# Kernel tuning notes

Hardware: AMD Instinct MI355X
Metric: run time of the kernel (lower is better)

The kernel has to match this reference:

```python
import jax, jax.numpy as jnp
import numpy as np

B, D, M, R, C = 1024, 32, 8, 4096, 32
TOPK_P = 0.1  # hard-coded in torch forward
EPS = 1e-9


def setup_inputs() -> dict:
    key = jax.random.key(0)
    k0, k1, k2, k3, k4 = jax.random.split(key, 5)
    x = jax.random.normal(k0, (B, D), dtype=jnp.float32)
    centers = jax.random.normal(k1, (D, M), dtype=jnp.float32)
    # widths kept away from 0 so gaussian MFs don't all underflow
    widths = jax.random.uniform(k2, (D, M), dtype=jnp.float32, minval=0.5, maxval=1.5)
    consequents = jax.random.uniform(k3, (R, D + 1, C), dtype=jnp.float32)
    rules = jax.random.randint(k4, (R, D), 0, M, dtype=jnp.int32)
    return {"x": x, "centers": centers, "widths": widths,
            "consequents": consequents, "rules": rules}


def reference(x, centers, widths, consequents, rules):
    Bn, Dn = x.shape
    Rn = rules.shape[0]
    # Gaussian membership functions: (B, D, M)
    mfs = jnp.exp(-((x[:, :, None] - centers[None]) ** 2) / (2.0 * widths[None] ** 2))
    # Gather per-rule MF values: (B, D, R)  (torch.gather along mf axis)
    rule_mfs = mfs[:, jnp.arange(Dn)[:, None], rules.T]
    # Firing strengths via product over input dims: (B, R)
    firing = jnp.prod(rule_mfs, axis=1)
    # top-K gate + scatter mask
    K = max(1, int(TOPK_P * Rn))
    _, idx = jax.lax.top_k(firing, K)
    mask = jnp.zeros_like(firing).at[jnp.arange(Bn)[:, None], idx].set(1.0)
    firing = firing * mask
    norm_fs = firing / (firing.sum(axis=1, keepdims=True) + EPS)
    # zeroG=False branch. Torch does einsum('bi,rjc->brc', x_ext, consequents)
    # which sums i and j independently: rule_mfs[b,r,c] = sum_i(x_ext[b,i]) * sum_j(cons[r,j,c]).
    # Then einsum('br,brc->bc') => out = sum(x_ext,1) * (norm_fs @ sum(cons,1)).
    x_ext_sum = x.sum(axis=1) + 1.0          # sum over x_ext = [x, 1], shape (B,)
    cons_sum = consequents.sum(axis=1)       # (R, C)
    rule_outputs = x_ext_sum[:, None] * (norm_fs @ cons_sum)  # (B, C)
    return rule_outputs, norm_fs, mask
```

## Files before the change

kernel.cpp:

```cpp
#include <hip/hip_runtime.h>

#define Bn 1024
#define Dn 32
#define Mn 8
#define Rn 4096
#define Cn 32
#define Kn 409
#define NTH 512
#define NBIN 1024
#define CCAP 256

typedef unsigned int u32;
typedef unsigned short u16;
typedef short bf16x8 __attribute__((ext_vector_type(8)));
typedef float f32x4 __attribute__((ext_vector_type(4)));

__device__ __forceinline__ int binof(float kf) {
    int b = (int)floorf(kf * (float)(NBIN / 120.0) + (float)NBIN);
    return b < 0 ? 0 : (b > NBIN - 1 ? NBIN - 1 : b);
}

__device__ __forceinline__ u16 f2bf(float v) {
    u32 b = __float_as_uint(v);
    b += 0x7fffu + ((b >> 16) & 1u);
    return (u16)(b >> 16);
}

__global__ __launch_bounds__(256) void prep_kernel(
    const float* __restrict__ x, const float* __restrict__ centers,
    const float* __restrict__ widths, const float* __restrict__ cons,
    const int* __restrict__ rules,
    float* __restrict__ cons_out,
    uint4* __restrict__ S4, uint4* __restrict__ Ehi4, uint4* __restrict__ Elo4)
{
    const int blk = blockIdx.x;
    const int t = threadIdx.x;
    if (blk < 512) {
        const int idx = blk * 256 + t;
        const int r = idx >> 5, c = idx & 31;
        const float* p = cons + (size_t)r * (Dn + 1) * Cn + c;
        float s = 0.0f;
#pragma unroll
        for (int k = 0; k < Dn + 1; ++k) s += p[(size_t)k * Cn];
        cons_out[idx] = s;
    } else if (blk < 1024) {
        const int r = (blk - 512) * 8 + (t >> 5);
        const int d = t & 31;
        const int v = rules[r * Dn + d];
        uint4 o;
        o.x = (v == 0 ? 0x3F80u : 0u) | (v == 1 ? (0x3F80u << 16) : 0u);
        o.y = (v == 2 ? 0x3F80u : 0u) | (v == 3 ? (0x3F80u << 16) : 0u);
        o.z = (v == 4 ? 0x3F80u : 0u) | (v == 5 ? (0x3F80u << 16) : 0u);
        o.w = (v == 6 ? 0x3F80u : 0u) | (v == 7 ? (0x3F80u << 16) : 0u);
        S4[r * 32 + d] = o;
    } else {
        const int row = (blk - 1024) * 8 + (t >> 5);
        const int d = t & 31;
        const float xv = x[row * Dn + d];
        u16 h[8], l[8];
#pragma unroll
        for (int m = 0; m < 8; ++m) {
            const float c = centers[d * 8 + m];
            const float w = widths[d * 8 + m];
            const float dx = xv - c;
            const float e = -(dx * dx) / (2.f * w * w);
            const u16 hb = f2bf(e);
            h[m] = hb;
            l[m] = f2bf(e - __uint_as_float((u32)hb << 16));
        }
        Ehi4[row * 32 + d] = make_uint4((u32)h[0] | ((u32)h[1] << 16), (u32)h[2] | ((u32)h[3] << 16),
                                        (u32)h[4] | ((u32)h[5] << 16), (u32)h[6] | ((u32)h[7] << 16));
        Elo4[row * 32 + d] = make_uint4((u32)l[0] | ((u32)l[1] << 16), (u32)l[2] | ((u32)l[3] << 16),
                                        (u32)l[4] | ((u32)l[5] << 16), (u32)l[6] | ((u32)l[7] << 16));
    }
}

__global__ __launch_bounds__(256) void key_gemm_kernel(
    const u16* __restrict__ Ehi, const u16* __restrict__ Elo,
    const u16* __restrict__ S, float* __restrict__ keys)
{
    __shared__ u16 sAh[2][64 * 32];
    __shared__ u16 sAl[2][64 * 32];
    __shared__ u16 sB[2][128 * 32];
    const int t = threadIdx.x;
    const int lane = t & 63;
    const int w = t >> 6;
    const int wr = w >> 1, wc = w & 1;
    const int m0 = blockIdx.y * 64;
    const int n0 = blockIdx.x * 128;

    f32x4 acc[2][4];
#pragma unroll
    for (int i = 0; i < 2; ++i)
#pragma unroll
        for (int j = 0; j < 4; ++j) acc[i][j] = (f32x4){0.f, 0.f, 0.f, 0.f};

    const int rowA = t >> 2;
    const int rowB1 = t >> 2;
    const int rowB2 = (t + 256) >> 2;
    const int koff = (t & 3) * 8;

#define GLDS(src, dst) __builtin_amdgcn_global_load_lds( \
        (const __attribute__((address_space(1))) void*)(src), \
        (__attribute__((address_space(3))) void*)(dst), 16, 0, 0)
#define STAGE(buf, k0) do { \
        GLDS(Ehi + (size_t)(m0 + rowA) * 256 + (k0) + koff, sAh[buf] + t * 8); \
        GLDS(Elo + (size_t)(m0 + rowA) * 256 + (k0) + koff, sAl[buf] + t * 8); \
        GLDS(S + (size_t)(n0 + rowB1) * 256 + (k0) + koff, sB[buf] + t * 8); \
        GLDS(S + (size_t)(n0 + rowB2) * 256 + (k0) + koff, sB[buf] + (t + 256) * 8); \
    } while (0)

    STAGE(0, 0);
    __syncthreads();
    int cur = 0;
    for (int k0 = 0; k0 < 256; k0 += 32) {
        if (k0 + 32 < 256) STAGE(cur ^ 1, k0 + 32);
        bf16x8 ah[2], al[2], b[4];
#pragma unroll
        for (int mi = 0; mi < 2; ++mi) {
            ah[mi] = *(const bf16x8*)(sAh[cur] + ((wr * 32 + mi * 16 + (lane & 15)) * 32 + (lane >> 4) * 8));
            al[mi] = *(const bf16x8*)(sAl[cur] + ((wr * 32 + mi * 16 + (lane & 15)) * 32 + (lane >> 4) * 8));
        }
#pragma unroll
        for (int ni = 0; ni < 4; ++ni)
            b[ni] = *(const bf16x8*)(sB[cur] + ((wc * 64 + ni * 16 + (lane & 15)) * 32 + (lane >> 4) * 8));
#pragma unroll
        for (int mi = 0; mi < 2; ++mi)
#pragma unroll
            for (int ni = 0; ni < 4; ++ni) {
                acc[mi][ni] = __builtin_amdgcn_mfma_f32_16x16x32_bf16(ah[mi], b[ni], acc[mi][ni], 0, 0, 0);
                acc[mi][ni] = __builtin_amdgcn_mfma_f32_16x16x32_bf16(al[mi], b[ni], acc[mi][ni], 0, 0, 0);
            }
        __syncthreads();
        cur ^= 1;
    }
#undef STAGE
#undef GLDS

    const int cr = (lane >> 4) * 4;
    const int cc = lane & 15;
#pragma unroll
    for (int mi = 0; mi < 2; ++mi)
#pragma unroll
        for (int ni = 0; ni < 4; ++ni)
#pragma unroll
            for (int reg = 0; reg < 4; ++reg)
                keys[(size_t)(m0 + wr * 32 + mi * 16 + cr + reg) * Rn + (n0 + wc * 64 + ni * 16 + cc)] =
                    acc[mi][ni][reg];
}

__global__ __launch_bounds__(NTH, 8) void select_kernel(
    const float* __restrict__ x,
    const float* __restrict__ centers,
    const float* __restrict__ widths,
    const float* __restrict__ keys,
    const int* __restrict__ rules,
    const float* __restrict__ cons_sum,
    float* __restrict__ out_rule,
    float* __restrict__ out_norm,
    float* __restrict__ out_mask)
{
    __shared__ float  s_x[Dn];
    __shared__ double s_e[256];
    __shared__ u32    s_hist[NBIN + 2];
    __shared__ u32    s_selmask[Rn / 32];
    __shared__ int    s_wtot[8];
    __shared__ float  s_wsum[8];
    __shared__ int    s_wpre[8];
    __shared__ int    s_cidx[CCAP];
    __shared__ double s_cval[CCAP];
    __shared__ int    s_selidx[Kn + 8];
    __shared__ float  s_selv[Kn + 8];
    __shared__ float  s_red[NTH];
    __shared__ int    s_bb, s_ccnt;

    const int t = threadIdx.x;
    const int lane = t & 63;
    const int w = t >> 6;
    const int b = blockIdx.x;

    const f32x4* kptr = (const f32x4*)(keys + (size_t)b * Rn);
    f32x4 ka = kptr[t];
    f32x4 kb = kptr[NTH + t];

    if (t < Dn) s_x[t] = x[b * Dn + t];
    if (t == 0) { s_ccnt = 0; s_hist[NBIN] = 0u; s_hist[NBIN + 1] = 0u; }
    s_hist[t] = 0u;
    s_hist[t + NTH] = 0u;
    if (t < Rn / 32) s_selmask[t] = 0u;
    __syncthreads();

    if (t < 256) {
        const int d = t >> 3;
        const double dx = (double)s_x[d] - (double)centers[t];
        const double ww = (double)widths[t];
        s_e[t] = -(dx * dx) / (2.0 * (ww * ww));
    }
    atomicAdd(&s_hist[binof(ka.x)], 1u);
    atomicAdd(&s_hist[binof(ka.y)], 1u);
    atomicAdd(&s_hist[binof(ka.z)], 1u);
    atomicAdd(&s_hist[binof(ka.w)], 1u);
    atomicAdd(&s_hist[binof(kb.x)], 1u);
    atomicAdd(&s_hist[binof(kb.y)], 1u);
    atomicAdd(&s_hist[binof(kb.z)], 1u);
    atomicAdd(&s_hist[binof(kb.w)], 1u);
    __syncthreads();

    const int h0 = (int)s_hist[2 * t];
    const int h1 = (int)s_hist[2 * t + 1];
    const int loc = h0 + h1;
    int S = loc;
#pragma unroll
    for (int off = 1; off < 64; off <<= 1) {
        const int vv = __shfl(S, lane + off < 64 ? lane + off : lane);
        if (lane + off < 64) S += vv;
    }
    if (lane == 0) s_wtot[w] = S;
    __syncthreads();
    int wsuf = 0;
#pragma unroll
    for (int ww = 0; ww < 8; ++ww) wsuf += (ww > w) ? s_wtot[ww] : 0;
    const int full = S + wsuf;
    s_hist[2 * t] = (u32)full;
    s_hist[2 * t + 1] = (u32)(full - h0);
    if (full - loc < Kn && full >= Kn) {
        s_bb = (full - h0 >= Kn) ? (2 * t + 1) : (2 * t);
    }
    __syncthreads();
    const int bb = s_bb;
    const int hi = (bb + 1 > NBIN - 1) ? NBIN - 1 : bb + 1;
    const int lo = (bb - 1 < 0) ? 0 : bb - 1;
    const int Acnt = (int)s_hist[hi + 1];
    const int want_in = Kn - Acnt;

#define CAND(kf, ridx) { const int bn = binof(kf); \
        if (bn >= lo && bn <= hi) { const int pos = atomicAdd(&s_ccnt, 1); \
            if (pos < CCAP) s_cidx[pos] = (ridx); } }
    CAND(ka.x, 4 * t + 0) CAND(ka.y, 4 * t + 1) CAND(ka.z, 4 * t + 2) CAND(ka.w, 4 * t + 3)
    CAND(kb.x, 2048 + 4 * t + 0) CAND(kb.y, 2048 + 4 * t + 1)
    CAND(kb.z, 2048 + 4 * t + 2) CAND(kb.w, 2048 + 4 * t + 3)
#undef CAND
    __syncthreads();
    const int cnt = s_ccnt < CCAP ? s_ccnt : CCAP;
    if (t < cnt) {
        const int* rp = rules + s_cidx[t] * Dn;
        double s = 0.0;
#pragma unroll
        for (int d = 0; d < Dn; ++d) s += s_e[d * 8 + rp[d]];
        s_cval[t] = s;
    }
    __syncthreads();
    if (t < cnt) {
        const double mv = s_cval[t];
        const int mi = s_cidx[t];
        int rank = 0;
        for (int j = 0; j < cnt; ++j) {
            const double ov = s_cval[j];
            const int oi = s_cidx[j];
            rank += ((ov > mv) || (ov == mv && oi < mi)) ? 1 : 0;
        }
        if (rank < want_in) atomicOr(&s_selmask[mi >> 5], 1u << (mi & 31));
    }
    __syncthreads();

    u32 selbits = 0u;
    int cnt_sel = 0;
    float lsum = 0.f;
#define SEL(kf, ridx, bit) { const int bn = binof(kf); \
        bool sel = (bn > hi); \
        if (!sel && bn >= lo) sel = (s_selmask[(ridx) >> 5] >> ((ridx) & 31)) & 1u; \
        float f = 0.f; \
        if (sel) { f = expf(kf); selbits |= (1u << (bit)); ++cnt_sel; lsum += f; } \
        kf = f; }
    SEL(ka.x, 4 * t + 0, 0) SEL(ka.y, 4 * t + 1, 1) SEL(ka.z, 4 * t + 2, 2) SEL(ka.w, 4 * t + 3, 3)
    SEL(kb.x, 2048 + 4 * t + 0, 4) SEL(kb.y, 2048 + 4 * t + 1, 5)
    SEL(kb.z, 2048 + 4 * t + 2, 6) SEL(kb.w, 2048 + 4 * t + 3, 7)
#undef SEL
#pragma unroll
    for (int off = 32; off >= 1; off >>= 1) lsum += __shfl_xor(lsum, off);
    if (lane == 0) s_wsum[w] = lsum;
    int p = cnt_sel;
#pragma unroll
    for (int off = 1; off < 64; off <<= 1) {
        const int u = __shfl(p, lane >= off ? lane - off : lane);
        if (lane >= off) p += u;
    }
    if (lane == 63) s_wpre[w] = p;
    __syncthreads();
    float denom = 1e-9f;
#pragma unroll
    for (int ww = 0; ww < 8; ++ww) denom += s_wsum[ww];
    const float rinv = 1.0f / denom;
    int base = 0, nsel = 0;
#pragma unroll
    for (int ww = 0; ww < 8; ++ww) { base += (ww < w) ? s_wpre[ww] : 0; nsel += s_wpre[ww]; }
    int pos = base + (p - cnt_sel);

#define CPT(fv, ridx, bit) if ((selbits >> (bit)) & 1u) { s_selidx[pos] = (ridx); s_selv[pos] = fv; ++pos; }
    CPT(ka.x, 4 * t + 0, 0) CPT(ka.y, 4 * t + 1, 1) CPT(ka.z, 4 * t + 2, 2) CPT(ka.w, 4 * t + 3, 3)
    CPT(kb.x, 2048 + 4 * t + 0, 4) CPT(kb.y, 2048 + 4 * t + 1, 5)
    CPT(kb.z, 2048 + 4 * t + 2, 6) CPT(kb.w, 2048 + 4 * t + 3, 7)
#undef CPT

    {
        f32x4* onorm = (f32x4*)(out_norm + (size_t)b * Rn);
        f32x4* omask = (f32x4*)(out_mask + (size_t)b * Rn);
        f32x4 nv, mk;
        nv.x = ka.x * rinv; mk.x = (selbits & 1u) ? 1.f : 0.f;
        nv.y = ka.y * rinv; mk.y = (selbits & 2u) ? 1.f : 0.f;
        nv.z = ka.z * rinv; mk.z = (selbits & 4u) ? 1.f : 0.f;
        nv.w = ka.w * rinv; mk.w = (selbits & 8u) ? 1.f : 0.f;
        __builtin_nontemporal_store(nv, &onorm[t]);
        __builtin_nontemporal_store(mk, &omask[t]);
        nv.x = kb.x * rinv; mk.x = (selbits & 16u) ? 1.f : 0.f;
        nv.y = kb.y * rinv; mk.y = (selbits & 32u) ? 1.f : 0.f;
        nv.z = kb.z * rinv; mk.z = (selbits & 64u) ? 1.f : 0.f;
        nv.w = kb.w * rinv; mk.w = (selbits & 128u) ? 1.f : 0.f;
        __builtin_nontemporal_store(nv, &onorm[NTH + t]);
        __builtin_nontemporal_store(mk, &omask[NTH + t]);
    }
    __syncthreads();

    const int g = t >> 5;
    const int c = t & 31;
    float acc = 0.f;
    for (int i = g; i < nsel; i += 16) {
        acc += s_selv[i] * cons_sum[s_selidx[i] * Cn + c];
    }
    s_red[t] = acc;
    __syncthreads();
    if (t < Cn) {
        float ss = 0.f;
#pragma unroll
        for (int gg = 0; gg < 16; ++gg) ss += s_red[gg * 32 + t];
        float xs = 1.f;
#pragma unroll
        for (int d = 0; d < Dn; ++d) xs += s_x[d];
        __builtin_nontemporal_store(xs * ss * rinv, &out_rule[(size_t)b * Cn + t]);
    }
}

extern "C" void kernel_launch(void* const* d_in, const int* in_sizes, int n_in,
                              void* d_out, int out_size, void* d_ws, size_t ws_size,
                              hipStream_t stream) {
    (void)in_sizes; (void)n_in; (void)out_size; (void)ws_size;
    const float* x = (const float*)d_in[0];
    const float* centers = (const float*)d_in[1];
    const float* widths = (const float*)d_in[2];
    const float* consequents = (const float*)d_in[3];
    const int* rules = (const int*)d_in[4];

    float* out_rule = (float*)d_out;
    float* out_norm = out_rule + (size_t)Bn * Cn;
    float* out_mask = out_norm + (size_t)Bn * Rn;

    char* wsb = (char*)d_ws;
    float* cons_sum = (float*)wsb;
    u16*   Smat  = (u16*)(wsb + (512 << 10));
    u16*   Ehi   = (u16*)(wsb + (2560 << 10));
    u16*   Elo   = (u16*)(wsb + (3072 << 10));
    float* keys  = (float*)(wsb + (3584 << 10));

    prep_kernel<<<1152, 256, 0, stream>>>(x, centers, widths, consequents, rules,
                                          cons_sum, (uint4*)Smat, (uint4*)Ehi, (uint4*)Elo);
    dim3 gg(Rn / 128, Bn / 64);
    key_gemm_kernel<<<gg, 256, 0, stream>>>(Ehi, Elo, Smat, keys);
    select_kernel<<<Bn, NTH, 0, stream>>>(x, centers, widths, keys, rules, cons_sum,
                                          out_rule, out_norm, out_mask);
}
```

Before: 42.60 us.

## Fuse prep stage into key GEMM, building operands on the fly in LDS

Removes the separate prep kernel. The GEMM blocks now compute the log-membership hi/lo bf16 split and the one-hot rule matrix directly into shared memory, and also accumulate the consequent sums. This cuts one launch and the global round trip for Ehi/Elo/S. In exchange, operand construction is recomputed redundantly across blocks, and the double-buffered async global-to-LDS pipeline becomes single-buffered with compute and MFMA serialized between barriers.

After: 43.22 us. Within noise of the previous version (+1.5%).

```diff
diff --git a/kernel.cpp b/kernel.cpp
--- a/kernel.cpp
+++ b/kernel.cpp
@@ -26,62 +26,27 @@
     return (u16)(b >> 16);
 }
 
-__global__ __launch_bounds__(256) void prep_kernel(
+__device__ __forceinline__ uint4 onehot4(int v) {
+    uint4 o;
+    o.x = (v == 0 ? 0x3F80u : 0u) | (v == 1 ? (0x3F80u << 16) : 0u);
+    o.y = (v == 2 ? 0x3F80u : 0u) | (v == 3 ? (0x3F80u << 16) : 0u);
+    o.z = (v == 4 ? 0x3F80u : 0u) | (v == 5 ? (0x3F80u << 16) : 0u);
+    o.w = (v == 6 ? 0x3F80u : 0u) | (v == 7 ? (0x3F80u << 16) : 0u);
+    return o;
+}
+
+__global__ __launch_bounds__(256) void fused_gemm_kernel(
     const float* __restrict__ x, const float* __restrict__ centers,
     const float* __restrict__ widths, const float* __restrict__ cons,
     const int* __restrict__ rules,
-    float* __restrict__ cons_out,
-    uint4* __restrict__ S4, uint4* __restrict__ Ehi4, uint4* __restrict__ Elo4)
+    float* __restrict__ cons_out, float* __restrict__ keys)
 {
-    const int blk = blockIdx.x;
-    const int t = threadIdx.x;
-    if (blk < 512) {
-        const int idx = blk * 256 + t;
-        const int r = idx >> 5, c = idx & 31;
-        const float* p = cons + (size_t)r * (Dn + 1) * Cn + c;
-        float s = 0.0f;
-#pragma unroll
-        for (int k = 0; k < Dn + 1; ++k) s += p[(size_t)k * Cn];
-        cons_out[idx] = s;
-    } else if (blk < 1024) {
-        const int r = (blk - 512) * 8 + (t >> 5);
-        const int d = t & 31;
-        const int v = rules[r * Dn + d];
-        uint4 o;
-        o.x = (v == 0 ? 0x3F80u : 0u) | (v == 1 ? (0x3F80u << 16) : 0u);
-        o.y = (v == 2 ? 0x3F80u : 0u) | (v == 3 ? (0x3F80u << 16) : 0u);
-        o.z = (v == 4 ? 0x3F80u : 0u) | (v == 5 ? (0x3F80u << 16) : 0u);
-        o.w = (v == 6 ? 0x3F80u : 0u) | (v == 7 ? (0x3F80u << 16) : 0u);
-        S4[r * 32 + d] = o;
-    } else {
-        const int row = (blk - 1024) * 8 + (t >> 5);
-        const int d = t & 31;
-        const float xv = x[row * Dn + d];
-        u16 h[8], l[8];
-#pragma unroll
-        for (int m = 0; m < 8; ++m) {
-            const float c = centers[d * 8 + m];
-            const float w = widths[d * 8 + m];
-            const float dx = xv - c;
-            const float e = -(dx * dx) / (2.f * w * w);
-            const u16 hb = f2bf(e);
-            h[m] = hb;
-            l[m] = f2bf(e - __uint_as_float((u32)hb << 16));
-        }
-        Ehi4[row * 32 + d] = make_uint4((u32)h[0] | ((u32)h[1] << 16), (u32)h[2] | ((u32)h[3] << 16),
-                                        (u32)h[4] | ((u32)h[5] << 16), (u32)h[6] | ((u32)h[7] << 16));
-        Elo4[row * 32 + d] = make_uint4((u32)l[0] | ((u32)l[1] << 16), (u32)l[2] | ((u32)l[3] << 16),
-                                        (u32)l[4] | ((u32)l[5] << 16), (u32)l[6] | ((u32)l[7] << 16));
-    }
-}
-
-__global__ __launch_bounds__(256) void key_gemm_kernel(
-    const u16* __restrict__ Ehi, const u16* __restrict__ Elo,
-    const u16* __restrict__ S, float* __restrict__ keys)
-{
-    __shared__ u16 sAh[2][64 * 32];
-    __shared__ u16 sAl[2][64 * 32];
-    __shared__ u16 sB[2][128 * 32];
+    __shared__ u16 sAh[64 * 32];
+    __shared__ u16 sAl[64 * 32];
+    __shared__ u16 sB[128 * 32];
+    __shared__ float s_cen[256];
+    __shared__ float s_inv[256];
+
     const int t = threadIdx.x;
     const int lane = t & 63;
     const int w = t >> 6;
@@ -89,41 +54,66 @@
     const int m0 = blockIdx.y * 64;
     const int n0 = blockIdx.x * 128;
 
+    {
+        const float ww = widths[t];
+        s_cen[t] = centers[t];
+        s_inv[t] = 0.5f / (ww * ww);
+    }
+
+    const int cidx = (blockIdx.y * 32 + blockIdx.x) * 256 + t;
+    const float* cp = cons + (size_t)(cidx >> 5) * ((Dn + 1) * Cn) + (cidx & 31);
+    float csum = 0.f;
+
     f32x4 acc[2][4];
 #pragma unroll
     for (int i = 0; i < 2; ++i)
 #pragma unroll
         for (int j = 0; j < 4; ++j) acc[i][j] = (f32x4){0.f, 0.f, 0.f, 0.f};
 
-    const int rowA = t >> 2;
-    const int rowB1 = t >> 2;
-    const int rowB2 = (t + 256) >> 2;
-    const int koff = (t & 3) * 8;
-
-#define GLDS(src, dst) __builtin_amdgcn_global_load_lds( \
-        (const __attribute__((address_space(1))) void*)(src), \
-        (__attribute__((address_space(3))) void*)(dst), 16, 0, 0)
-#define STAGE(buf, k0) do { \
-        GLDS(Ehi + (size_t)(m0 + rowA) * 256 + (k0) + koff, sAh[buf] + t * 8); \
-        GLDS(Elo + (size_t)(m0 + rowA) * 256 + (k0) + koff, sAl[buf] + t * 8); \
-        GLDS(S + (size_t)(n0 + rowB1) * 256 + (k0) + koff, sB[buf] + t * 8); \
-        GLDS(S + (size_t)(n0 + rowB2) * 256 + (k0) + koff, sB[buf] + (t + 256) * 8); \
-    } while (0)
-
-    STAGE(0, 0);
-    __syncthreads();
-    int cur = 0;
-    for (int k0 = 0; k0 < 256; k0 += 32) {
-        if (k0 + 32 < 256) STAGE(cur ^ 1, k0 + 32);
+    const int arow = t >> 2;
+    const int aj = t & 3;
+    __syncthreads();
+
+    for (int ki = 0; ki < 8; ++ki) {
+        const int d0 = ki * 4;
+        {
+            const int v0 = rules[(n0 + arow) * Dn + d0 + aj];
+            const int v1 = rules[(n0 + 64 + arow) * Dn + d0 + aj];
+            *(uint4*)(sB + arow * 32 + aj * 8) = onehot4(v0);
+            *(uint4*)(sB + (64 + arow) * 32 + aj * 8) = onehot4(v1);
+        }
+        {
+            const float xv = x[(m0 + arow) * Dn + d0 + aj];
+            const int dm0 = (d0 + aj) * 8;
+            u16 h[8], l[8];
+#pragma unroll
+            for (int m = 0; m < 8; ++m) {
+                const float dx = xv - s_cen[dm0 + m];
+                const float e = -(dx * dx) * s_inv[dm0 + m];
+                const u16 hb = f2bf(e);
+                h[m] = hb;
+                l[m] = f2bf(e - __uint_as_float((u32)hb << 16));
+            }
+            *(uint4*)(sAh + arow * 32 + aj * 8) =
+                make_uint4((u32)h[0] | ((u32)h[1] << 16), (u32)h[2] | ((u32)h[3] << 16),
+                           (u32)h[4] | ((u32)h[5] << 16), (u32)h[6] | ((u32)h[7] << 16));
+            *(uint4*)(sAl + arow * 32 + aj * 8) =
+                make_uint4((u32)l[0] | ((u32)l[1] << 16), (u32)l[2] | ((u32)l[3] << 16),
+                           (u32)l[4] | ((u32)l[5] << 16), (u32)l[6] | ((u32)l[7] << 16));
+        }
+#pragma unroll
+        for (int u = 0; u < 4; ++u) csum += cp[(ki * 4 + u) * Cn];
+
+        __syncthreads();
         bf16x8 ah[2], al[2], b[4];
 #pragma unroll
         for (int mi = 0; mi < 2; ++mi) {
-            ah[mi] = *(const bf16x8*)(sAh[cur] + ((wr * 32 + mi * 16 + (lane & 15)) * 32 + (lane >> 4) * 8));
-            al[mi] = *(const bf16x8*)(sAl[cur] + ((wr * 32 + mi * 16 + (lane & 15)) * 32 + (lane >> 4) * 8));
+            ah[mi] = *(const bf16x8*)(sAh + ((wr * 32 + mi * 16 + (lane & 15)) * 32 + (lane >> 4) * 8));
+            al[mi] = *(const bf16x8*)(sAl + ((wr * 32 + mi * 16 + (lane & 15)) * 32 + (lane >> 4) * 8));
         }
 #pragma unroll
         for (int ni = 0; ni < 4; ++ni)
-            b[ni] = *(const bf16x8*)(sB[cur] + ((wc * 64 + ni * 16 + (lane & 15)) * 32 + (lane >> 4) * 8));
+            b[ni] = *(const bf16x8*)(sB + ((wc * 64 + ni * 16 + (lane & 15)) * 32 + (lane >> 4) * 8));
 #pragma unroll
         for (int mi = 0; mi < 2; ++mi)
 #pragma unroll
@@ -132,10 +122,9 @@
                 acc[mi][ni] = __builtin_amdgcn_mfma_f32_16x16x32_bf16(al[mi], b[ni], acc[mi][ni], 0, 0, 0);
             }
         __syncthreads();
-        cur ^= 1;
-    }
-#undef STAGE
-#undef GLDS
+    }
+    csum += cp[Dn * Cn];
+    cons_out[cidx] = csum;
 
     const int cr = (lane >> 4) * 4;
     const int cc = lane & 15;
@@ -356,15 +345,11 @@
 
     char* wsb = (char*)d_ws;
     float* cons_sum = (float*)wsb;
-    u16*   Smat  = (u16*)(wsb + (512 << 10));
-    u16*   Ehi   = (u16*)(wsb + (2560 << 10));
-    u16*   Elo   = (u16*)(wsb + (3072 << 10));
-    float* keys  = (float*)(wsb + (3584 << 10));
-
-    prep_kernel<<<1152, 256, 0, stream>>>(x, centers, widths, consequents, rules,
-                                          cons_sum, (uint4*)Smat, (uint4*)Ehi, (uint4*)Elo);
+    float* keys = (float*)(wsb + (512 << 10));
+
     dim3 gg(Rn / 128, Bn / 64);
-    key_gemm_kernel<<<gg, 256, 0, stream>>>(Ehi, Elo, Smat, keys);
+    fused_gemm_kernel<<<gg, 256, 0, stream>>>(x, centers, widths, consequents, rules,
+                                              cons_sum, keys);
     select_kernel<<<Bn, NTH, 0, stream>>>(x, centers, widths, keys, rules, cons_sum,
                                           out_rule, out_norm, out_mask);
 }
```
